# Kernel tuning notes

Measured on AMD Instinct MI355X. Metric: run time of the kernel, lower is better.

The kernel has to match this reference:

```python
import jax, jax.numpy as jnp
import numpy as np

N_QUBITS = 7
N_LAYERS = 5
DIM = 2 ** N_QUBITS  # 128


def _apply_1q(state, U, q):
    """Apply single-qubit gate U ((2,2) shared or (B,2,2) per-sample) on wire q.
    state: (B, 2,2,2,2,2,2,2), wire 0 = most significant axis (PennyLane order)."""
    state = jnp.moveaxis(state, 1 + q, -1)
    if U.ndim == 2:
        state = state @ U.T
    else:
        state = jnp.einsum('bij,b...j->b...i', U, state)
    return jnp.moveaxis(state, -1, 1 + q)


def _apply_cnot(state, c, t):
    state = jnp.moveaxis(state, (1 + c, 1 + t), (-2, -1))
    new = jnp.stack([state[..., 0, :], state[..., 1, ::-1]], axis=-2)
    return jnp.moveaxis(new, (-2, -1), (1 + c, 1 + t))


def _rot_matrix(phi, theta, omega):
    # PennyLane Rot(phi, theta, omega) = RZ(omega) @ RY(theta) @ RZ(phi)
    c = jnp.cos(theta / 2)
    s = jnp.sin(theta / 2)
    ep = jnp.exp(-0.5j * (phi + omega))
    em = jnp.exp(0.5j * (phi - omega))
    row0 = jnp.stack([ep * c, -em * s])
    row1 = jnp.stack([jnp.conj(em) * s, jnp.conj(ep) * c])
    return jnp.stack([row0, row1]).astype(jnp.complex64)


def _simulate(x, qweights):
    B = x.shape[0]
    state = jnp.zeros((B, DIM), jnp.complex64).at[:, 0].set(1.0)
    state = state.reshape((B,) + (2,) * N_QUBITS)
    # AngleEmbedding rotation='Y': RY(x_q) on wire q, per-sample angles
    c = jnp.cos(x / 2)
    s = jnp.sin(x / 2)
    for q in range(N_QUBITS):
        U = jnp.stack([jnp.stack([c[:, q], -s[:, q]], -1),
                       jnp.stack([s[:, q], c[:, q]], -1)], -2).astype(jnp.complex64)
        state = _apply_1q(state, U, q)
    # StronglyEntanglingLayers: Rot on each wire, then ring of CNOTs with range r
    for l in range(N_LAYERS):
        r = l % (N_QUBITS - 1) + 1
        for q in range(N_QUBITS):
            state = _apply_1q(state, _rot_matrix(qweights[l, q, 0], qweights[l, q, 1], qweights[l, q, 2]), q)
        for q in range(N_QUBITS):
            state = _apply_cnot(state, q, (q + r) % N_QUBITS)
    # expval(PauliZ(q)) for each wire
    probs = (state.real ** 2 + state.imag ** 2).reshape(B, DIM)
    idx = jnp.arange(DIM)
    bits = (idx[None, :] >> (N_QUBITS - 1 - jnp.arange(N_QUBITS))[:, None]) & 1  # (7,128)
    signs = (1 - 2 * bits).astype(probs.dtype)
    return probs @ signs.T  # (B, 7)


def setup_inputs() -> dict:
    key = jax.random.key(0)
    ks = jax.random.split(key, 6)
    B, n_classes = 32768, 22
    x = jax.random.normal(ks[0], (B, N_QUBITS), dtype=jnp.float32)
    qweights = jax.random.uniform(ks[1], (N_LAYERS, N_QUBITS, 3), dtype=jnp.float32,
                                  minval=0.0, maxval=2.0 * np.pi)
    W1 = jax.random.normal(ks[2], (16, N_QUBITS), dtype=jnp.float32) / np.sqrt(N_QUBITS)
    b1 = jax.random.normal(ks[3], (16,), dtype=jnp.float32) * 0.01
    W2 = jax.random.normal(ks[4], (n_classes, 16), dtype=jnp.float32) / 4.0
    b2 = jax.random.normal(ks[5], (n_classes,), dtype=jnp.float32) * 0.01
    return {"x": x, "qweights": qweights, "W1": W1, "b1": b1, "W2": W2, "b2": b2}


def reference(x, qweights, W1, b1, W2, b2):
    q_out = _simulate(x, qweights)              # (B, 7) real expvals
    h = jax.nn.relu(q_out @ W1.T + b1)          # (B, 16)
    # Dropout(p=0.3) is identity in eval mode
    logits = h @ W2.T + b2                      # (B, 22)
    return logits
```

## Files before the change

kernel.cpp:

```cpp
#include <hip/hip_runtime.h>
#include <math.h>

#define DIM 128

typedef __attribute__((ext_vector_type(8))) short bf16x8;
typedef __attribute__((ext_vector_type(4))) float f32x4;

static __device__ __forceinline__ unsigned short f2bf(float v) {
  unsigned u = __float_as_uint(v);
  unsigned r = (u + 0x7FFFu + ((u >> 16) & 1u)) >> 16;
  return (unsigned short)r;
}
static __device__ __forceinline__ float bf2f(unsigned short u) {
  return __uint_as_float(((unsigned)u) << 16);
}

__global__ __launch_bounds__(256) void build_unitary_k(
    const float* __restrict__ qw, unsigned short* __restrict__ Bhi,
    unsigned short* __restrict__ Blo) {
  __shared__ float gm[35][8];
  const int tid = threadIdx.x;

  if (tid < 35) {
    const float phi = qw[tid * 3 + 0];
    const float th  = qw[tid * 3 + 1];
    const float om  = qw[tid * 3 + 2];
    float sh, ch; sincosf(0.5f * th, &sh, &ch);
    const float a = 0.5f * (phi + om);
    const float b = 0.5f * (phi - om);
    float sa, ca; sincosf(a, &sa, &ca);
    float sb, cb; sincosf(b, &sb, &cb);
    gm[tid][0] =  ca * ch;  gm[tid][1] = -sa * ch;
    gm[tid][2] = -cb * sh;  gm[tid][3] = -sb * sh;
    gm[tid][4] =  cb * sh;  gm[tid][5] = -sb * sh;
    gm[tid][6] =  ca * ch;  gm[tid][7] =  sa * ch;
  }
  __syncthreads();

  const int lane = tid & 63;
  const int k    = blockIdx.x * 4 + (tid >> 6);

  float rl = (k == lane)      ? 1.f : 0.f;
  float rh = (k == lane + 64) ? 1.f : 0.f;
  float il = 0.f, ih = 0.f;

  for (int l = 0; l < 5; ++l) {
    const int r = l % 6 + 1;
    for (int q = 0; q < 7; ++q) {
      const float* g = gm[l * 7 + q];
      const float g0 = g[0], g1 = g[1], g2 = g[2], g3 = g[3];
      const float g4 = g[4], g5 = g[5], g6 = g[6], g7 = g[7];
      if (q == 0) {
        const float nrl = g0 * rl - g1 * il + g2 * rh - g3 * ih;
        const float nil = g0 * il + g1 * rl + g2 * ih + g3 * rh;
        const float nrh = g4 * rl - g5 * il + g6 * rh - g7 * ih;
        const float nih = g4 * il + g5 * rl + g6 * ih + g7 * rh;
        rl = nrl; il = nil; rh = nrh; ih = nih;
      } else {
        const int m = 1 << (6 - q);
        const int bit = (lane & m) ? 1 : 0;
        const float prl = __shfl_xor(rl, m), pil = __shfl_xor(il, m);
        const float prh = __shfl_xor(rh, m), pih = __shfl_xor(ih, m);
        const float udr = bit ? g6 : g0, udi = bit ? g7 : g1;
        const float uor = bit ? g4 : g2, uoi = bit ? g5 : g3;
        const float nrl = udr * rl - udi * il + uor * prl - uoi * pil;
        const float nil = udr * il + udi * rl + uor * pil + uoi * prl;
        const float nrh = udr * rh - udi * ih + uor * prh - uoi * pih;
        const float nih = udr * ih + udi * rh + uor * pih + uoi * prh;
        rl = nrl; il = nil; rh = nrh; ih = nih;
      }
    }
    for (int q = 0; q < 7; ++q) {
      const int tg = (q + r) % 7;
      if (q == 0) {
        const int mt = 1 << (6 - tg);
        const float prh = __shfl_xor(rh, mt), pih = __shfl_xor(ih, mt);
        rh = prh; ih = pih;
      } else if (tg == 0) {
        const int mc = 1 << (6 - q);
        const bool cb = (lane & mc) != 0;
        const float trl = cb ? rh : rl, til = cb ? ih : il;
        const float trh = cb ? rl : rh, tih = cb ? il : ih;
        rl = trl; il = til; rh = trh; ih = tih;
      } else {
        const int mc = 1 << (6 - q), mt = 1 << (6 - tg);
        const bool cb = (lane & mc) != 0;
        const float prl = __shfl_xor(rl, mt), pil = __shfl_xor(il, mt);
        const float prh = __shfl_xor(rh, mt), pih = __shfl_xor(ih, mt);
        rl = cb ? prl : rl; il = cb ? pil : il;
        rh = cb ? prh : rh; ih = cb ? pih : ih;
      }
    }
  }

  const int kt = k >> 5, kl = (k >> 3) & 3, e = k & 7;
  {
    const float vals[4] = {rl, rh, il, ih};
    #pragma unroll
    for (int t = 0; t < 4; ++t) {
      const int n = lane + t * 64;
      const int off = (((n >> 4) * 4 + kt) * 64 + kl * 16 + (n & 15)) * 8 + e;
      const unsigned short h = f2bf(vals[t]);
      Bhi[off] = h;
      Blo[off] = f2bf(vals[t] - bf2f(h));
    }
  }
}

__global__ __launch_bounds__(512, 4) void vqc_mlp_k(
    const float* __restrict__ x,
    const unsigned short* __restrict__ Bhi, const unsigned short* __restrict__ Blo,
    const float* __restrict__ W1, const float* __restrict__ b1,
    const float* __restrict__ W2, const float* __restrict__ b2,
    float* __restrict__ out) {
  __shared__ unsigned short Ahi[32 * 136];
  __shared__ unsigned short Alo[32 * 136];
  __shared__ float qaP[8 * 32 * 8];
  const int tid  = threadIdx.x;
  const int lane = tid & 63;
  const int w    = tid >> 6;
  const int s0   = blockIdx.x * 32;

  const bf16x8* __restrict__ Bh8 = (const bf16x8*)Bhi;
  const bf16x8* __restrict__ Bl8 = (const bf16x8*)Blo;
  bf16x8 bh[2][4], bl[2][4];
  #pragma unroll
  for (int t = 0; t < 2; ++t) {
    const int ct = w + t * 8;
    #pragma unroll
    for (int kt = 0; kt < 4; ++kt) {
      bh[t][kt] = Bh8[(ct * 4 + kt) * 64 + lane];
      bl[t][kt] = Bl8[(ct * 4 + kt) * 64 + lane];
    }
  }

  {
    const int sam = tid >> 4;
    const int ko  = tid & 15;
    const float* xp = x + (s0 + sam) * 7;
    float cq[7], sq[7];
    #pragma unroll
    for (int q = 0; q < 7; ++q) sincosf(0.5f * xp[q], &sq[q], &cq[q]);
    float sv[8];
    sv[0] = ((ko & 8) ? sq[0] : cq[0]) * ((ko & 4) ? sq[1] : cq[1]) *
            ((ko & 2) ? sq[2] : cq[2]) * ((ko & 1) ? sq[3] : cq[3]);
    #pragma unroll
    for (int q = 4; q < 7; ++q) {
      const int cnt = 1 << (q - 4);
      #pragma unroll
      for (int t2 = cnt - 1; t2 >= 0; --t2) {
        const float v = sv[t2];
        sv[2 * t2 + 1] = v * sq[q];
        sv[2 * t2]     = v * cq[q];
      }
    }
    bf16x8 h8, l8;
    #pragma unroll
    for (int e = 0; e < 8; ++e) {
      const unsigned short h = f2bf(sv[e]);
      h8[e] = (short)h;
      l8[e] = (short)f2bf(sv[e] - bf2f(h));
    }
    *(bf16x8*)&Ahi[sam * 136 + ko * 8] = h8;
    *(bf16x8*)&Alo[sam * 136 + ko * 8] = l8;
  }
  __syncthreads();

  f32x4 acc00 = {0.f, 0.f, 0.f, 0.f};
  f32x4 acc01 = {0.f, 0.f, 0.f, 0.f};
  f32x4 acc10 = {0.f, 0.f, 0.f, 0.f};
  f32x4 acc11 = {0.f, 0.f, 0.f, 0.f};
  const int r0 = (lane & 15) * 136;
  const int r1 = (16 + (lane & 15)) * 136;
  const int kloff = (lane >> 4) * 8;
  #pragma unroll
  for (int kt = 0; kt < 4; ++kt) {
    const int ko2 = kt * 32 + kloff;
    const bf16x8 ah0 = *(const bf16x8*)&Ahi[r0 + ko2];
    const bf16x8 al0 = *(const bf16x8*)&Alo[r0 + ko2];
    const bf16x8 ah1 = *(const bf16x8*)&Ahi[r1 + ko2];
    const bf16x8 al1 = *(const bf16x8*)&Alo[r1 + ko2];
    acc00 = __builtin_amdgcn_mfma_f32_16x16x32_bf16(ah0, bh[0][kt], acc00, 0, 0, 0);
    acc01 = __builtin_amdgcn_mfma_f32_16x16x32_bf16(ah0, bh[1][kt], acc01, 0, 0, 0);
    acc10 = __builtin_amdgcn_mfma_f32_16x16x32_bf16(ah1, bh[0][kt], acc10, 0, 0, 0);
    acc11 = __builtin_amdgcn_mfma_f32_16x16x32_bf16(ah1, bh[1][kt], acc11, 0, 0, 0);
    acc00 = __builtin_amdgcn_mfma_f32_16x16x32_bf16(ah0, bl[0][kt], acc00, 0, 0, 0);
    acc01 = __builtin_amdgcn_mfma_f32_16x16x32_bf16(ah0, bl[1][kt], acc01, 0, 0, 0);
    acc10 = __builtin_amdgcn_mfma_f32_16x16x32_bf16(ah1, bl[0][kt], acc10, 0, 0, 0);
    acc11 = __builtin_amdgcn_mfma_f32_16x16x32_bf16(ah1, bl[1][kt], acc11, 0, 0, 0);
    acc00 = __builtin_amdgcn_mfma_f32_16x16x32_bf16(al0, bh[0][kt], acc00, 0, 0, 0);
    acc01 = __builtin_amdgcn_mfma_f32_16x16x32_bf16(al0, bh[1][kt], acc01, 0, 0, 0);
    acc10 = __builtin_amdgcn_mfma_f32_16x16x32_bf16(al1, bh[0][kt], acc10, 0, 0, 0);
    acc11 = __builtin_amdgcn_mfma_f32_16x16x32_bf16(al1, bh[1][kt], acc11, 0, 0, 0);
  }

  const int c  = lane & 15;
  const int lg = lane >> 4;
  float u[2][4][5];
  #pragma unroll
  for (int st = 0; st < 2; ++st) {
    const f32x4 yr = (st == 0) ? acc00 : acc10;
    const f32x4 yi = (st == 0) ? acc01 : acc11;
    #pragma unroll
    for (int r = 0; r < 4; ++r) {
      const float p = yr[r] * yr[r] + yi[r] * yi[r];
      #pragma unroll
      for (int a = 0; a < 5; ++a) u[st][r][a] = p;
    }
  }
  #pragma unroll
  for (int stg = 0; stg < 4; ++stg) {
    const int m = 8 >> stg;
    const int di = stg + 1;
    #pragma unroll
    for (int st = 0; st < 2; ++st)
      #pragma unroll
      for (int r = 0; r < 4; ++r)
        #pragma unroll
        for (int a = 0; a < 5; ++a) {
          const float xv = __shfl_xor(u[st][r][a], m);
          if (a == di) u[st][r][a] = (c & m) ? (xv - u[st][r][a]) : (u[st][r][a] - xv);
          else         u[st][r][a] += xv;
        }
  }
  const int sg0 = (w >> 2) & 1, sg1 = (w >> 1) & 1, sg2 = w & 1;
  if (c < 7) {
    #pragma unroll
    for (int st = 0; st < 2; ++st)
      #pragma unroll
      for (int r = 0; r < 4; ++r) {
        const float u0 = u[st][r][0];
        float v;
        if (c == 0)      v = sg0 ? -u0 : u0;
        else if (c == 1) v = sg1 ? -u0 : u0;
        else if (c == 2) v = sg2 ? -u0 : u0;
        else if (c == 3) v = u[st][r][1];
        else if (c == 4) v = u[st][r][2];
        else if (c == 5) v = u[st][r][3];
        else             v = u[st][r][4];
        qaP[w * 256 + (st * 16 + lg * 4 + r) * 8 + c] = v;
      }
  }
  __syncthreads();

  if (tid < 352) {
    const int s  = tid / 11;
    const int oo = tid - s * 11;
    float qv[7];
    #pragma unroll
    for (int q = 0; q < 7; ++q) {
      float a2 = 0.f;
      #pragma unroll
      for (int wv = 0; wv < 8; ++wv) a2 += qaP[wv * 256 + s * 8 + q];
      qv[q] = a2;
    }
    float h[16];
    #pragma unroll
    for (int k = 0; k < 16; ++k) {
      float a2 = b1[k];
      #pragma unroll
      for (int q = 0; q < 7; ++q) a2 += W1[k * 7 + q] * qv[q];
      h[k] = fmaxf(a2, 0.f);
    }
    #pragma unroll
    for (int oi = 0; oi < 2; ++oi) {
      const int o = oo + oi * 11;
      float lg2 = b2[o];
      #pragma unroll
      for (int k = 0; k < 16; ++k) lg2 += W2[o * 16 + k] * h[k];
      out[(s0 + s) * 22 + o] = lg2;
    }
  }
}

extern "C" void kernel_launch(void* const* d_in, const int* in_sizes, int n_in,
                              void* d_out, int out_size, void* d_ws, size_t ws_size,
                              hipStream_t stream) {
  const float* x  = (const float*)d_in[0];
  const float* qw = (const float*)d_in[1];
  const float* W1 = (const float*)d_in[2];
  const float* b1 = (const float*)d_in[3];
  const float* W2 = (const float*)d_in[4];
  const float* b2 = (const float*)d_in[5];
  float* out = (float*)d_out;
  unsigned short* Bhi = (unsigned short*)d_ws;
  unsigned short* Blo = Bhi + 128 * 256;

  const int B = in_sizes[0] / 7;

  build_unitary_k<<<32, 256, 0, stream>>>(qw, Bhi, Blo);

  vqc_mlp_k<<<B / 32, 512, 0, stream>>>(x, Bhi, Blo, W1, b1, W2, b2, out);
}
```

Before: 92.06 us.

## Transpose MFMA operands to cut shuffle reduction and alias shared buffers

Swaps the A and B operands of the MFMA calls so each lane's four accumulator rows hold basis indices instead of samples. The Pauli-Z sums over those low bits can then be done in registers, leaving only a few cross-lane shuffles in place of the old four-stage butterfly over 40 values. Shared memory is merged into one aliased buffer. The per-wave partial sums are reduced once into a compact array rather than by each of 352 threads, and sincosf becomes __sincosf. This adds two more barriers, and the fast sincos is less accurate for large inputs.

```diff
diff --git a/kernel.cpp b/kernel.cpp
--- a/kernel.cpp
+++ b/kernel.cpp
@@ -113,9 +113,12 @@
     const float* __restrict__ W1, const float* __restrict__ b1,
     const float* __restrict__ W2, const float* __restrict__ b2,
     float* __restrict__ out) {
-  __shared__ unsigned short Ahi[32 * 136];
-  __shared__ unsigned short Alo[32 * 136];
-  __shared__ float qaP[8 * 32 * 8];
+  __shared__ float smem[4608];
+  unsigned short* Ahi = (unsigned short*)smem;
+  unsigned short* Alo = (unsigned short*)(smem + 2176);
+  float* qaP = smem;
+  float* QA  = smem + 2304;
+
   const int tid  = threadIdx.x;
   const int lane = tid & 63;
   const int w    = tid >> 6;
@@ -140,7 +143,7 @@
     const float* xp = x + (s0 + sam) * 7;
     float cq[7], sq[7];
     #pragma unroll
-    for (int q = 0; q < 7; ++q) sincosf(0.5f * xp[q], &sq[q], &cq[q]);
+    for (int q = 0; q < 7; ++q) __sincosf(0.5f * xp[q], &sq[q], &cq[q]);
     float sv[8];
     sv[0] = ((ko & 8) ? sq[0] : cq[0]) * ((ko & 4) ? sq[1] : cq[1]) *
             ((ko & 2) ? sq[2] : cq[2]) * ((ko & 1) ? sq[3] : cq[3]);
@@ -180,66 +183,67 @@
     const bf16x8 al0 = *(const bf16x8*)&Alo[r0 + ko2];
     const bf16x8 ah1 = *(const bf16x8*)&Ahi[r1 + ko2];
     const bf16x8 al1 = *(const bf16x8*)&Alo[r1 + ko2];
-    acc00 = __builtin_amdgcn_mfma_f32_16x16x32_bf16(ah0, bh[0][kt], acc00, 0, 0, 0);
-    acc01 = __builtin_amdgcn_mfma_f32_16x16x32_bf16(ah0, bh[1][kt], acc01, 0, 0, 0);
-    acc10 = __builtin_amdgcn_mfma_f32_16x16x32_bf16(ah1, bh[0][kt], acc10, 0, 0, 0);
-    acc11 = __builtin_amdgcn_mfma_f32_16x16x32_bf16(ah1, bh[1][kt], acc11, 0, 0, 0);
-    acc00 = __builtin_amdgcn_mfma_f32_16x16x32_bf16(ah0, bl[0][kt], acc00, 0, 0, 0);
-    acc01 = __builtin_amdgcn_mfma_f32_16x16x32_bf16(ah0, bl[1][kt], acc01, 0, 0, 0);
-    acc10 = __builtin_amdgcn_mfma_f32_16x16x32_bf16(ah1, bl[0][kt], acc10, 0, 0, 0);
-    acc11 = __builtin_amdgcn_mfma_f32_16x16x32_bf16(ah1, bl[1][kt], acc11, 0, 0, 0);
-    acc00 = __builtin_amdgcn_mfma_f32_16x16x32_bf16(al0, bh[0][kt], acc00, 0, 0, 0);
-    acc01 = __builtin_amdgcn_mfma_f32_16x16x32_bf16(al0, bh[1][kt], acc01, 0, 0, 0);
-    acc10 = __builtin_amdgcn_mfma_f32_16x16x32_bf16(al1, bh[0][kt], acc10, 0, 0, 0);
-    acc11 = __builtin_amdgcn_mfma_f32_16x16x32_bf16(al1, bh[1][kt], acc11, 0, 0, 0);
-  }
-
-  const int c  = lane & 15;
-  const int lg = lane >> 4;
-  float u[2][4][5];
+    acc00 = __builtin_amdgcn_mfma_f32_16x16x32_bf16(bh[0][kt], ah0, acc00, 0, 0, 0);
+    acc01 = __builtin_amdgcn_mfma_f32_16x16x32_bf16(bh[1][kt], ah0, acc01, 0, 0, 0);
+    acc10 = __builtin_amdgcn_mfma_f32_16x16x32_bf16(bh[0][kt], ah1, acc10, 0, 0, 0);
+    acc11 = __builtin_amdgcn_mfma_f32_16x16x32_bf16(bh[1][kt], ah1, acc11, 0, 0, 0);
+    acc00 = __builtin_amdgcn_mfma_f32_16x16x32_bf16(bl[0][kt], ah0, acc00, 0, 0, 0);
+    acc01 = __builtin_amdgcn_mfma_f32_16x16x32_bf16(bl[1][kt], ah0, acc01, 0, 0, 0);
+    acc10 = __builtin_amdgcn_mfma_f32_16x16x32_bf16(bl[0][kt], ah1, acc10, 0, 0, 0);
+    acc11 = __builtin_amdgcn_mfma_f32_16x16x32_bf16(bl[1][kt], ah1, acc11, 0, 0, 0);
+    acc00 = __builtin_amdgcn_mfma_f32_16x16x32_bf16(bh[0][kt], al0, acc00, 0, 0, 0);
+    acc01 = __builtin_amdgcn_mfma_f32_16x16x32_bf16(bh[1][kt], al0, acc01, 0, 0, 0);
+    acc10 = __builtin_amdgcn_mfma_f32_16x16x32_bf16(bh[0][kt], al1, acc10, 0, 0, 0);
+    acc11 = __builtin_amdgcn_mfma_f32_16x16x32_bf16(bh[1][kt], al1, acc11, 0, 0, 0);
+  }
+
+  const int sg0 = (w >> 2) & 1, sg1 = (w >> 1) & 1, sg2 = w & 1;
+  float qv7[2][7];
   #pragma unroll
   for (int st = 0; st < 2; ++st) {
     const f32x4 yr = (st == 0) ? acc00 : acc10;
     const f32x4 yi = (st == 0) ? acc01 : acc11;
-    #pragma unroll
-    for (int r = 0; r < 4; ++r) {
-      const float p = yr[r] * yr[r] + yi[r] * yi[r];
-      #pragma unroll
-      for (int a = 0; a < 5; ++a) u[st][r][a] = p;
-    }
-  }
-  #pragma unroll
-  for (int stg = 0; stg < 4; ++stg) {
-    const int m = 8 >> stg;
-    const int di = stg + 1;
-    #pragma unroll
-    for (int st = 0; st < 2; ++st)
-      #pragma unroll
-      for (int r = 0; r < 4; ++r)
-        #pragma unroll
-        for (int a = 0; a < 5; ++a) {
-          const float xv = __shfl_xor(u[st][r][a], m);
-          if (a == di) u[st][r][a] = (c & m) ? (xv - u[st][r][a]) : (u[st][r][a] - xv);
-          else         u[st][r][a] += xv;
-        }
-  }
-  const int sg0 = (w >> 2) & 1, sg1 = (w >> 1) & 1, sg2 = w & 1;
-  if (c < 7) {
-    #pragma unroll
-    for (int st = 0; st < 2; ++st)
-      #pragma unroll
-      for (int r = 0; r < 4; ++r) {
-        const float u0 = u[st][r][0];
-        float v;
-        if (c == 0)      v = sg0 ? -u0 : u0;
-        else if (c == 1) v = sg1 ? -u0 : u0;
-        else if (c == 2) v = sg2 ? -u0 : u0;
-        else if (c == 3) v = u[st][r][1];
-        else if (c == 4) v = u[st][r][2];
-        else if (c == 5) v = u[st][r][3];
-        else             v = u[st][r][4];
-        qaP[w * 256 + (st * 16 + lg * 4 + r) * 8 + c] = v;
-      }
+    const float p0 = yr[0] * yr[0] + yi[0] * yi[0];
+    const float p1 = yr[1] * yr[1] + yi[1] * yi[1];
+    const float p2 = yr[2] * yr[2] + yi[2] * yi[2];
+    const float p3 = yr[3] * yr[3] + yi[3] * yi[3];
+    const float t  = p0 + p1 + p2 + p3;
+    const float d5 = p0 + p1 - p2 - p3;
+    const float d6 = p0 - p1 + p2 - p3;
+    const float t16 = __shfl_xor(t, 16);
+    const float a   = t + t16;
+    const float b4  = (lane & 16) ? (t16 - t) : (t - t16);
+    const float a32 = __shfl_xor(a, 32);
+    const float T   = a + a32;
+    const float D3  = (lane & 32) ? (a32 - a) : (a - a32);
+    const float D4  = b4 + __shfl_xor(b4, 32);
+    const float d5a = d5 + __shfl_xor(d5, 16);
+    const float D5  = d5a + __shfl_xor(d5a, 32);
+    const float d6a = d6 + __shfl_xor(d6, 16);
+    const float D6  = d6a + __shfl_xor(d6a, 32);
+    qv7[st][0] = sg0 ? -T : T;
+    qv7[st][1] = sg1 ? -T : T;
+    qv7[st][2] = sg2 ? -T : T;
+    qv7[st][3] = D3; qv7[st][4] = D4; qv7[st][5] = D5; qv7[st][6] = D6;
+  }
+  __syncthreads();
+
+  if (lane < 16) {
+    #pragma unroll
+    for (int st = 0; st < 2; ++st) {
+      const int base = w * 288 + (st * 16 + lane) * 9;
+      #pragma unroll
+      for (int q = 0; q < 7; ++q) qaP[base + q] = qv7[st][q];
+    }
+  }
+  __syncthreads();
+
+  if (tid < 224) {
+    const int q = tid >> 5, s = tid & 31;
+    float acc = 0.f;
+    #pragma unroll
+    for (int wv = 0; wv < 8; ++wv) acc += qaP[wv * 288 + s * 9 + q];
+    QA[s * 8 + q] = acc;
   }
   __syncthreads();
 
@@ -248,12 +252,7 @@
     const int oo = tid - s * 11;
     float qv[7];
     #pragma unroll
-    for (int q = 0; q < 7; ++q) {
-      float a2 = 0.f;
-      #pragma unroll
-      for (int wv = 0; wv < 8; ++wv) a2 += qaP[wv * 256 + s * 8 + q];
-      qv[q] = a2;
-    }
+    for (int q = 0; q < 7; ++q) qv[q] = QA[s * 8 + q];
     float h[16];
     #pragma unroll
     for (int k = 0; k < 16; ++k) {
```

Measured after the change: 82.37 us. 1.12x faster.
